# Kernel optimization log

Measured on AMD Instinct MI355X. Metric: run time of the kernel, lower is better.

Reference implementation:

```python
import jax, jax.numpy as jnp
import numpy as np

B, C_IN, N, HC = 32, 128, 8192, 64
HEAD_NAMES = ['hm', 'reg', 'height', 'dim', 'rot', 'iou']
HEAD_OUT = [3, 2, 1, 3, 2, 1]
EPS = 1e-5
INIT_BIAS = -2.19


def setup_inputs() -> dict:
    key = jax.random.key(0)
    ks = jax.random.split(key, 16)
    d = {}
    d['ct_feat'] = jax.random.normal(ks[0], (B, C_IN, N), jnp.float32)
    # shared conv (1x1) + BN1d params
    d['sh_w'] = jax.random.normal(ks[1], (HC, C_IN), jnp.float32) * 0.05
    d['sh_b'] = jnp.zeros((HC,), jnp.float32)
    d['sh_g'] = jnp.ones((HC,), jnp.float32)
    d['sh_beta'] = jnp.zeros((HC,), jnp.float32)
    d['sh_mean'] = jax.random.normal(ks[2], (HC,), jnp.float32) * 0.1
    d['sh_var'] = jax.random.uniform(ks[3], (HC,), jnp.float32) + 0.5
    # first conv layer of each SepHead branch (stacked over 6 heads)
    d['head_w1'] = jax.random.normal(ks[4], (6, HC, HC), jnp.float32) * 0.05
    d['head_b1'] = jnp.zeros((6, HC), jnp.float32)
    d['head_g1'] = jnp.ones((6, HC), jnp.float32)
    d['head_beta1'] = jnp.zeros((6, HC), jnp.float32)
    d['head_mean1'] = jax.random.normal(ks[5], (6, HC), jnp.float32) * 0.1
    d['head_var1'] = jax.random.uniform(ks[6], (6, HC), jnp.float32) + 0.5
    # final conv of each branch (distinct out channels)
    for i, (name, c_out) in enumerate(zip(HEAD_NAMES, HEAD_OUT)):
        d[name + '_w'] = jax.random.normal(ks[7 + i], (c_out, HC), jnp.float32) * 0.05
        if name == 'hm':  # hm final bias is filled with init_bias
            d[name + '_b'] = jnp.full((c_out,), INIT_BIAS, jnp.float32)
        else:
            d[name + '_b'] = jnp.zeros((c_out,), jnp.float32)
    return d


def _bn(x, g, b, m, v):
    # x: [B, C, N]; params: [C]
    return (x - m[:, None]) * jax.lax.rsqrt(v[:, None] + EPS) * g[:, None] + b[:, None]


def reference(ct_feat, sh_w, sh_b, sh_g, sh_beta, sh_mean, sh_var,
              head_w1, head_b1, head_g1, head_beta1, head_mean1, head_var1,
              hm_w, hm_b, reg_w, reg_b, height_w, height_b,
              dim_w, dim_b, rot_w, rot_b, iou_w, iou_b):
    # shared_conv: Conv1d(k=1) + BN1d + ReLU
    y = jnp.einsum('oc,bcn->bon', sh_w, ct_feat) + sh_b[:, None]
    y = jax.nn.relu(_bn(y, sh_g, sh_beta, sh_mean, sh_var))  # [B, HC, N]

    # first layer of all 6 head branches, batched over head axis h
    z = jnp.einsum('hoc,bcn->hbon', head_w1, y) + head_b1[:, None, :, None]
    z = (z - head_mean1[:, None, :, None]) * jax.lax.rsqrt(head_var1[:, None, :, None] + EPS)
    z = z * head_g1[:, None, :, None] + head_beta1[:, None, :, None]
    z = jax.nn.relu(z)  # [6, B, HC, N]

    finals = [(hm_w, hm_b), (reg_w, reg_b), (height_w, height_b),
              (dim_w, dim_b), (rot_w, rot_b), (iou_w, iou_b)]
    outs = [jnp.einsum('oc,bcn->bon', w, z[i]) + b[:, None]
            for i, (w, b) in enumerate(finals)]
    # concat in head order [hm(3), reg(2), height(1), dim(3), rot(2), iou(1)] -> [B, 12, N]
    return jnp.concatenate(outs, axis=1)
```

## Files before the change

kernel.cpp:

```cpp
#include <hip/hip_runtime.h>
#include <hip/hip_bf16.h>
#include <cstdint>

typedef __attribute__((ext_vector_type(8))) short bf16x8;
typedef __attribute__((ext_vector_type(4))) float f32x4;
typedef __attribute__((ext_vector_type(2))) int i32x2;

#define NCOL 8192

#define WS_AW 0
#define WS_A1 8192
#define WS_AF 32768
#define WS_U16_TOTAL 38912
#define WS_OFSH 19456
#define WS_OFH  19520
#define WS_BIAS 19904
#define PREP_TOTAL (WS_U16_TOTAL + 464)

union FragU { uint32_t u[4]; bf16x8 v; uint4 q; };

__device__ __forceinline__ uint16_t f2bf(float f) {
  uint32_t x = __builtin_bit_cast(uint32_t, f);
  x += 0x7fffu + ((x >> 16) & 1u);
  return (uint16_t)(x >> 16);
}
__device__ __forceinline__ uint32_t rne_bits(float f) {
  uint32_t x = __builtin_bit_cast(uint32_t, f);
  return x + 0x7fffu + ((x >> 16) & 1u);
}
__device__ __forceinline__ uint32_t pack_bf16(float lo, float hi) {
  return __builtin_amdgcn_perm(rne_bits(hi), rne_bits(lo), 0x07060302u);
}

__device__ __forceinline__ void cswap(uint32_t lo, uint32_t hi,
                                      uint32_t& f1, uint32_t& f2) {
  i32x2 t = __builtin_amdgcn_permlane32_swap((int)lo, (int)hi, false, false);
  i32x2 f = __builtin_amdgcn_permlane16_swap(t[0], t[1], false, false);
  f1 = (uint32_t)f[0];
  f2 = (uint32_t)f[1];
}

__global__ __launch_bounds__(256) void ch_prep(
    const float* __restrict__ shw, const float* __restrict__ shb,
    const float* __restrict__ shg, const float* __restrict__ shbeta,
    const float* __restrict__ shmean, const float* __restrict__ shvar,
    const float* __restrict__ w1, const float* __restrict__ b1,
    const float* __restrict__ g1, const float* __restrict__ beta1,
    const float* __restrict__ mean1, const float* __restrict__ var1,
    const float* __restrict__ hm_w, const float* __restrict__ hm_b,
    const float* __restrict__ reg_w, const float* __restrict__ reg_b,
    const float* __restrict__ height_w, const float* __restrict__ height_b,
    const float* __restrict__ dim_w, const float* __restrict__ dim_b,
    const float* __restrict__ rot_w, const float* __restrict__ rot_b,
    const float* __restrict__ iou_w, const float* __restrict__ iou_b,
    uint16_t* __restrict__ wsq)
{
  const int e = blockIdx.x * 256 + threadIdx.x;
  if (e >= PREP_TOTAL) return;
  const int rowbase[6] = {0, 3, 5, 6, 9, 11};
  const int couts[6]   = {3, 2, 1, 3, 2, 1};
  const float* wfp[6]  = {hm_w, reg_w, height_w, dim_w, rot_w, iou_w};

  if (e < WS_A1) {
    const int i = e & 7, q = (e >> 3) & 3, kc = (e >> 5) & 3, m = e >> 7;
    const int k = kc * 32 + q * 8 + i;
    const float sc = shg[m] * rsqrtf(shvar[m] + 1e-5f);
    wsq[e] = f2bf(shw[m * 128 + k] * sc);
  } else if (e < WS_AF) {
    const int e2 = e - WS_A1;
    const int i = e2 & 7, q = (e2 >> 3) & 3, kc = (e2 >> 5) & 1,
              m = (e2 >> 6) & 63, h = e2 >> 12;
    const int k = kc * 32 + q * 8 + i, row = h * 64 + m;
    const float sc = g1[row] * rsqrtf(var1[row] + 1e-5f);
    wsq[e] = f2bf(w1[row * 64 + k] * sc);
  } else if (e < WS_U16_TOTAL) {
    const int e2 = e - WS_AF;
    const int i = e2 & 7, q = (e2 >> 3) & 3, kc = (e2 >> 5) & 1,
              m = (e2 >> 6) & 15, h = e2 >> 10;
    const int k = kc * 32 + q * 8 + i, rr = m - rowbase[h];
    const float v = (rr >= 0 && rr < couts[h]) ? wfp[h][rr * 64 + k] : 0.f;
    wsq[e] = f2bf(v);
  } else {
    const int t2 = e - WS_U16_TOTAL;
    float* wff = (float*)wsq;
    float v = 0.f;
    if (t2 < 64) {
      const float sc = shg[t2] * rsqrtf(shvar[t2] + 1e-5f);
      v = (shb[t2] - shmean[t2]) * sc + shbeta[t2];
    } else if (t2 < 448) {
      const int i = t2 - 64;
      const float sc = g1[i] * rsqrtf(var1[i] + 1e-5f);
      v = (b1[i] - mean1[i]) * sc + beta1[i];
    } else {
      const int i = t2 - 448;
      if (i < 3)       v = hm_b[i];
      else if (i < 5)  v = reg_b[i - 3];
      else if (i < 6)  v = height_b[i - 5];
      else if (i < 9)  v = dim_b[i - 6];
      else if (i < 11) v = rot_b[i - 9];
      else if (i < 12) v = iou_b[i - 11];
    }
    wff[WS_OFSH + t2] = v;
  }
}

__global__ __launch_bounds__(256) void ch_main(
    const float* __restrict__ ct,
    const uint16_t* __restrict__ wsq,
    const float* __restrict__ wsf,
    float* __restrict__ outp)
{
  const int t    = threadIdx.x;
  const int wv   = t >> 6;
  const int lane = t & 63;
  const int l15  = lane & 15;
  const int qd   = lane >> 4;
  const int bid  = blockIdx.x;
  const int b    = bid >> 6;
  const int col0 = (bid & 63) * 128;
  const int nb   = wv * 32;

  const float* ctb = ct + (size_t)b * 128 * NCOL;
  const int voff0 = qd * 8 * NCOL + col0 + nb + l15;

  float xv[4][2][8];
  #pragma unroll
  for (int kc = 0; kc < 4; ++kc)
    #pragma unroll
    for (int j = 0; j < 2; ++j)
      #pragma unroll
      for (int i2 = 0; i2 < 4; ++i2) {
        const size_t off = (size_t)((kc * 32 + 2 * i2) * NCOL) + voff0 + j * 16;
        xv[kc][j][2 * i2]     = ctb[off];
        xv[kc][j][2 * i2 + 1] = ctb[off + NCOL];
      }
  __builtin_amdgcn_sched_barrier(0);

  f32x4 accY[4][2];
  #pragma unroll
  for (int mt = 0; mt < 4; ++mt)
    #pragma unroll
    for (int j = 0; j < 2; ++j)
      accY[mt][j] = (f32x4){0.f, 0.f, 0.f, 0.f};

  #pragma unroll
  for (int kc = 0; kc < 4; ++kc) {
    bf16x8 a[4];
    #pragma unroll
    for (int mt = 0; mt < 4; ++mt) {
      FragU fa;
      fa.q = *(const uint4*)(wsq + WS_AW + ((mt * 16 + l15) * 4 + kc) * 32 + qd * 8);
      a[mt] = fa.v;
    }
    #pragma unroll
    for (int j = 0; j < 2; ++j) {
      FragU f;
      #pragma unroll
      for (int i2 = 0; i2 < 4; ++i2)
        f.u[i2] = pack_bf16(xv[kc][j][2 * i2], xv[kc][j][2 * i2 + 1]);
      #pragma unroll
      for (int mt = 0; mt < 4; ++mt)
        accY[mt][j] = __builtin_amdgcn_mfma_f32_16x16x32_bf16(a[mt], f.v, accY[mt][j], 0, 0, 0);
    }
  }

  FragU yfrag[2][2];
  #pragma unroll
  for (int j = 0; j < 2; ++j) {
    uint32_t P[4][2];
    #pragma unroll
    for (int mt = 0; mt < 4; ++mt) {
      const f32x4 of = *(const f32x4*)(wsf + WS_OFSH + mt * 16 + qd * 4);
      const f32x4 v = accY[mt][j];
      P[mt][0] = pack_bf16(fmaxf(v[0] + of[0], 0.f), fmaxf(v[1] + of[1], 0.f));
      P[mt][1] = pack_bf16(fmaxf(v[2] + of[2], 0.f), fmaxf(v[3] + of[3], 0.f));
    }
    #pragma unroll
    for (int kc = 0; kc < 2; ++kc)
      #pragma unroll
      for (int u = 0; u < 2; ++u)
        cswap(P[2 * kc][u], P[2 * kc + 1][u],
              yfrag[kc][j].u[u], yfrag[kc][j].u[u + 2]);
  }

  f32x4 accO[2];
  accO[0] = (f32x4){0.f, 0.f, 0.f, 0.f};
  accO[1] = (f32x4){0.f, 0.f, 0.f, 0.f};

  const uint16_t* a1p = wsq + WS_A1 + l15 * 64 + qd * 8;
  const uint16_t* afp = wsq + WS_AF + l15 * 64 + qd * 8;
  const float*    ofp = wsf + WS_OFH + qd * 4;

  #pragma unroll 1
  for (int h = 0; h < 6; ++h) {
    FragU wa[2][4];
    FragU af[2];
    f32x4 ofv[4];
    #pragma unroll
    for (int kc = 0; kc < 2; ++kc)
      #pragma unroll
      for (int mt = 0; mt < 4; ++mt)
        wa[kc][mt].q = *(const uint4*)(a1p + mt * 1024 + kc * 32);
    #pragma unroll
    for (int kc = 0; kc < 2; ++kc)
      af[kc].q = *(const uint4*)(afp + kc * 32);
    #pragma unroll
    for (int mt = 0; mt < 4; ++mt)
      ofv[mt] = *(const f32x4*)(ofp + mt * 16);
    __builtin_amdgcn_sched_barrier(0);

    f32x4 accZ[4][2];
    #pragma unroll
    for (int mt = 0; mt < 4; ++mt)
      #pragma unroll
      for (int j = 0; j < 2; ++j)
        accZ[mt][j] = (f32x4){0.f, 0.f, 0.f, 0.f};

    #pragma unroll
    for (int kc = 0; kc < 2; ++kc)
      #pragma unroll
      for (int j = 0; j < 2; ++j)
        #pragma unroll
        for (int mt = 0; mt < 4; ++mt)
          accZ[mt][j] = __builtin_amdgcn_mfma_f32_16x16x32_bf16(wa[kc][mt].v, yfrag[kc][j].v, accZ[mt][j], 0, 0, 0);

    #pragma unroll
    for (int j = 0; j < 2; ++j) {
      uint32_t Q[4][2];
      #pragma unroll
      for (int mt = 0; mt < 4; ++mt) {
        const f32x4 v = accZ[mt][j];
        Q[mt][0] = pack_bf16(fmaxf(v[0] + ofv[mt][0], 0.f), fmaxf(v[1] + ofv[mt][1], 0.f));
        Q[mt][1] = pack_bf16(fmaxf(v[2] + ofv[mt][2], 0.f), fmaxf(v[3] + ofv[mt][3], 0.f));
      }
      FragU zf[2];
      #pragma unroll
      for (int kc = 0; kc < 2; ++kc)
        #pragma unroll
        for (int u = 0; u < 2; ++u)
          cswap(Q[2 * kc][u], Q[2 * kc + 1][u], zf[kc].u[u], zf[kc].u[u + 2]);

      #pragma unroll
      for (int kc = 0; kc < 2; ++kc)
        accO[j] = __builtin_amdgcn_mfma_f32_16x16x32_bf16(af[kc].v, zf[kc].v, accO[j], 0, 0, 0);
    }

    a1p += 4096;
    afp += 1024;
    ofp += 64;
  }

  if (qd < 3) {
    const f32x4 bs = *(const f32x4*)(wsf + WS_BIAS + qd * 4);
    #pragma unroll
    for (int j = 0; j < 2; ++j) {
      const int col = col0 + nb + j * 16 + l15;
      #pragma unroll
      for (int r = 0; r < 4; ++r)
        outp[((size_t)(b * 12 + qd * 4 + r)) * NCOL + col] = accO[j][r] + bs[r];
    }
  }
}

extern "C" void kernel_launch(void* const* d_in, const int* in_sizes, int n_in,
                              void* d_out, int out_size, void* d_ws, size_t ws_size,
                              hipStream_t stream) {
  (void)out_size; (void)ws_size;
  static const int sortedPos[25] = {
      0, 24, 19, 21, 20, 22, 23, 8, 3, 5, 4, 6, 7,
      12, 11, 16, 15, 10, 9, 2, 1, 18, 17, 14, 13};
  const bool sorted_order =
      (n_in == 25) && (in_sizes[1] == 3) && (in_sizes[2] == 192) &&
      (in_sizes[8] == 24576) && (in_sizes[24] == 8192);
  const float* p[25];
  for (int r = 0; r < 25; ++r)
    p[r] = (const float*)d_in[sorted_order ? sortedPos[r] : r];

  uint16_t* wsq = (uint16_t*)d_ws;

  hipLaunchKernelGGL(ch_prep, dim3((PREP_TOTAL + 255) / 256), dim3(256), 0, stream,
      p[1], p[2], p[3], p[4], p[5], p[6],
      p[7], p[8], p[9], p[10], p[11], p[12],
      p[13], p[14], p[15], p[16], p[17], p[18],
      p[19], p[20], p[21], p[22], p[23], p[24],
      wsq);

  hipLaunchKernelGGL(ch_main, dim3(2048), dim3(256), 0, stream,
      p[0], (const uint16_t*)wsq, (const float*)wsq, (float*)d_out);
}
```

Baseline: 292.6 us.

## Double-buffer input tiles in LDS via async global_load_lds with persistent column loop

The main kernel now has each block process 8 consecutive 64-column tiles instead of one 128-column tile. Input tiles are staged into a double-buffered, XOR-swizzled LDS buffer with asynchronous global-to-LDS loads, so the next tile's fetch overlaps the current tile's MFMA work. Shared-conv weights and offsets are hoisted out of the loop into registers, and the grid shrinks to 512 blocks with launch bounds asking for 2 blocks per CU. The trade-off is 64KB of LDS per block and hand-written vmcnt waits, which cap occupancy and depend on the exact count of outstanding loads.

```diff
diff --git a/kernel.cpp b/kernel.cpp
--- a/kernel.cpp
+++ b/kernel.cpp
@@ -104,132 +104,143 @@
   }
 }
 
-__global__ __launch_bounds__(256) void ch_main(
+__global__ __launch_bounds__(256, 2) void ch_main(
     const float* __restrict__ ct,
     const uint16_t* __restrict__ wsq,
     const float* __restrict__ wsf,
     float* __restrict__ outp)
 {
+  __shared__ __align__(16) float sm_x[2][128 * 64];
+
   const int t    = threadIdx.x;
   const int wv   = t >> 6;
   const int lane = t & 63;
   const int l15  = lane & 15;
   const int qd   = lane >> 4;
   const int bid  = blockIdx.x;
-  const int b    = bid >> 6;
-  const int col0 = (bid & 63) * 128;
-  const int nb   = wv * 32;
-
+  const int b    = bid >> 4;
+  const int g    = bid & 15;
   const float* ctb = ct + (size_t)b * 128 * NCOL;
-  const int voff0 = qd * 8 * NCOL + col0 + nb + l15;
-
-  float xv[4][2][8];
+
+#define STAGE(bsel, it)                                                        \
+  {                                                                            \
+    const int col0_ = (g * 8 + (it)) * 64;                                     \
+    _Pragma("unroll")                                                          \
+    for (int i = 0; i < 8; ++i) {                                              \
+      const int ii = wv * 8 + i;                                               \
+      const int k  = 4 * ii + qd;                                              \
+      const int sw = (k >> 3) & 3;                                             \
+      const float* src = ctb + (size_t)k * NCOL + col0_ +                      \
+                         ((4 * l15) ^ (sw << 4));                              \
+      __builtin_amdgcn_global_load_lds(                                        \
+          (const __attribute__((address_space(1))) uint32_t*)src,              \
+          (__attribute__((address_space(3))) uint32_t*)&sm_x[bsel][ii * 256],  \
+          16, 0, 0);                                                           \
+    }                                                                          \
+  }
+
+  FragU aw[4][4];
   #pragma unroll
   for (int kc = 0; kc < 4; ++kc)
     #pragma unroll
-    for (int j = 0; j < 2; ++j)
-      #pragma unroll
-      for (int i2 = 0; i2 < 4; ++i2) {
-        const size_t off = (size_t)((kc * 32 + 2 * i2) * NCOL) + voff0 + j * 16;
-        xv[kc][j][2 * i2]     = ctb[off];
-        xv[kc][j][2 * i2 + 1] = ctb[off + NCOL];
-      }
-  __builtin_amdgcn_sched_barrier(0);
-
-  f32x4 accY[4][2];
+    for (int mt = 0; mt < 4; ++mt)
+      aw[kc][mt].q = *(const uint4*)(wsq + WS_AW + ((mt * 16 + l15) * 4 + kc) * 32 + qd * 8);
+  f32x4 ofsh[4];
   #pragma unroll
   for (int mt = 0; mt < 4; ++mt)
-    #pragma unroll
-    for (int j = 0; j < 2; ++j)
-      accY[mt][j] = (f32x4){0.f, 0.f, 0.f, 0.f};
-
-  #pragma unroll
-  for (int kc = 0; kc < 4; ++kc) {
-    bf16x8 a[4];
-    #pragma unroll
-    for (int mt = 0; mt < 4; ++mt) {
-      FragU fa;
-      fa.q = *(const uint4*)(wsq + WS_AW + ((mt * 16 + l15) * 4 + kc) * 32 + qd * 8);
-      a[mt] = fa.v;
-    }
-    #pragma unroll
-    for (int j = 0; j < 2; ++j) {
-      FragU f;
-      #pragma unroll
-      for (int i2 = 0; i2 < 4; ++i2)
-        f.u[i2] = pack_bf16(xv[kc][j][2 * i2], xv[kc][j][2 * i2 + 1]);
-      #pragma unroll
-      for (int mt = 0; mt < 4; ++mt)
-        accY[mt][j] = __builtin_amdgcn_mfma_f32_16x16x32_bf16(a[mt], f.v, accY[mt][j], 0, 0, 0);
-    }
-  }
-
-  FragU yfrag[2][2];
-  #pragma unroll
-  for (int j = 0; j < 2; ++j) {
-    uint32_t P[4][2];
-    #pragma unroll
-    for (int mt = 0; mt < 4; ++mt) {
-      const f32x4 of = *(const f32x4*)(wsf + WS_OFSH + mt * 16 + qd * 4);
-      const f32x4 v = accY[mt][j];
-      P[mt][0] = pack_bf16(fmaxf(v[0] + of[0], 0.f), fmaxf(v[1] + of[1], 0.f));
-      P[mt][1] = pack_bf16(fmaxf(v[2] + of[2], 0.f), fmaxf(v[3] + of[3], 0.f));
-    }
-    #pragma unroll
-    for (int kc = 0; kc < 2; ++kc)
-      #pragma unroll
-      for (int u = 0; u < 2; ++u)
-        cswap(P[2 * kc][u], P[2 * kc + 1][u],
-              yfrag[kc][j].u[u], yfrag[kc][j].u[u + 2]);
-  }
-
-  f32x4 accO[2];
-  accO[0] = (f32x4){0.f, 0.f, 0.f, 0.f};
-  accO[1] = (f32x4){0.f, 0.f, 0.f, 0.f};
-
-  const uint16_t* a1p = wsq + WS_A1 + l15 * 64 + qd * 8;
-  const uint16_t* afp = wsq + WS_AF + l15 * 64 + qd * 8;
-  const float*    ofp = wsf + WS_OFH + qd * 4;
+    ofsh[mt] = *(const f32x4*)(wsf + WS_OFSH + mt * 16 + qd * 4);
+  const f32x4 bs = *(const f32x4*)(wsf + WS_BIAS + (qd & 3) * 4);
+
+  STAGE(0, 0);
+  STAGE(1, 1);
 
   #pragma unroll 1
-  for (int h = 0; h < 6; ++h) {
-    FragU wa[2][4];
-    FragU af[2];
-    f32x4 ofv[4];
-    #pragma unroll
-    for (int kc = 0; kc < 2; ++kc)
-      #pragma unroll
-      for (int mt = 0; mt < 4; ++mt)
-        wa[kc][mt].q = *(const uint4*)(a1p + mt * 1024 + kc * 32);
-    #pragma unroll
-    for (int kc = 0; kc < 2; ++kc)
-      af[kc].q = *(const uint4*)(afp + kc * 32);
+  for (int it = 0; it < 8; ++it) {
+    const int bsel = it & 1;
+    const int col0 = (g * 8 + it) * 64;
+
+    if (it == 0)      asm volatile("s_waitcnt vmcnt(8)" ::: "memory");
+    else if (it < 7)  asm volatile("s_waitcnt vmcnt(12)" ::: "memory");
+    else              asm volatile("s_waitcnt vmcnt(0)" ::: "memory");
+    __builtin_amdgcn_s_barrier();
+
+    const float* smf = &sm_x[bsel][0];
+    const int cx = (wv * 16 + l15) ^ (qd << 4);
+
+    f32x4 accY[4];
     #pragma unroll
     for (int mt = 0; mt < 4; ++mt)
-      ofv[mt] = *(const f32x4*)(ofp + mt * 16);
-    __builtin_amdgcn_sched_barrier(0);
-
-    f32x4 accZ[4][2];
+      accY[mt] = (f32x4){0.f, 0.f, 0.f, 0.f};
+
     #pragma unroll
-    for (int mt = 0; mt < 4; ++mt)
-      #pragma unroll
-      for (int j = 0; j < 2; ++j)
-        accZ[mt][j] = (f32x4){0.f, 0.f, 0.f, 0.f};
-
-    #pragma unroll
-    for (int kc = 0; kc < 2; ++kc)
-      #pragma unroll
-      for (int j = 0; j < 2; ++j)
+    for (int kc = 0; kc < 4; ++kc) {
+      FragU f;
+      #pragma unroll
+      for (int i2 = 0; i2 < 4; ++i2) {
+        const int k = kc * 32 + qd * 8 + 2 * i2;
+        const int w = k * 64 + cx;
+        f.u[i2] = pack_bf16(smf[w], smf[w + 64]);
+      }
+      #pragma unroll
+      for (int mt = 0; mt < 4; ++mt)
+        accY[mt] = __builtin_amdgcn_mfma_f32_16x16x32_bf16(aw[kc][mt].v, f.v, accY[mt], 0, 0, 0);
+    }
+    __builtin_amdgcn_s_barrier();
+
+    if (it < 6) STAGE(bsel, it + 2);
+
+    FragU yfrag[2];
+    {
+      uint32_t P[4][2];
+      #pragma unroll
+      for (int mt = 0; mt < 4; ++mt) {
+        const f32x4 v = accY[mt];
+        P[mt][0] = pack_bf16(fmaxf(v[0] + ofsh[mt][0], 0.f), fmaxf(v[1] + ofsh[mt][1], 0.f));
+        P[mt][1] = pack_bf16(fmaxf(v[2] + ofsh[mt][2], 0.f), fmaxf(v[3] + ofsh[mt][3], 0.f));
+      }
+      #pragma unroll
+      for (int kc = 0; kc < 2; ++kc)
+        #pragma unroll
+        for (int u = 0; u < 2; ++u)
+          cswap(P[2 * kc][u], P[2 * kc + 1][u], yfrag[kc].u[u], yfrag[kc].u[u + 2]);
+    }
+
+    f32x4 accO = (f32x4){0.f, 0.f, 0.f, 0.f};
+    const uint16_t* a1p = wsq + WS_A1 + l15 * 64 + qd * 8;
+    const uint16_t* afp = wsq + WS_AF + l15 * 64 + qd * 8;
+    const float*    ofp = wsf + WS_OFH + qd * 4;
+
+    #pragma unroll 1
+    for (int h = 0; h < 6; ++h) {
+      FragU wa[2][4];
+      FragU af[2];
+      f32x4 ofv[4];
+      #pragma unroll
+      for (int kc = 0; kc < 2; ++kc)
         #pragma unroll
         for (int mt = 0; mt < 4; ++mt)
-          accZ[mt][j] = __builtin_amdgcn_mfma_f32_16x16x32_bf16(wa[kc][mt].v, yfrag[kc][j].v, accZ[mt][j], 0, 0, 0);
-
-    #pragma unroll
-    for (int j = 0; j < 2; ++j) {
+          wa[kc][mt].q = *(const uint4*)(a1p + mt * 1024 + kc * 32);
+      #pragma unroll
+      for (int kc = 0; kc < 2; ++kc)
+        af[kc].q = *(const uint4*)(afp + kc * 32);
+      #pragma unroll
+      for (int mt = 0; mt < 4; ++mt)
+        ofv[mt] = *(const f32x4*)(ofp + mt * 16);
+
+      f32x4 accZ[4];
+      #pragma unroll
+      for (int mt = 0; mt < 4; ++mt)
+        accZ[mt] = (f32x4){0.f, 0.f, 0.f, 0.f};
+      #pragma unroll
+      for (int kc = 0; kc < 2; ++kc)
+        #pragma unroll
+        for (int mt = 0; mt < 4; ++mt)
+          accZ[mt] = __builtin_amdgcn_mfma_f32_16x16x32_bf16(wa[kc][mt].v, yfrag[kc].v, accZ[mt], 0, 0, 0);
+
       uint32_t Q[4][2];
       #pragma unroll
       for (int mt = 0; mt < 4; ++mt) {
-        const f32x4 v = accZ[mt][j];
+        const f32x4 v = accZ[mt];
         Q[mt][0] = pack_bf16(fmaxf(v[0] + ofv[mt][0], 0.f), fmaxf(v[1] + ofv[mt][1], 0.f));
         Q[mt][1] = pack_bf16(fmaxf(v[2] + ofv[mt][2], 0.f), fmaxf(v[3] + ofv[mt][3], 0.f));
       }
@@ -239,27 +250,23 @@
         #pragma unroll
         for (int u = 0; u < 2; ++u)
           cswap(Q[2 * kc][u], Q[2 * kc + 1][u], zf[kc].u[u], zf[kc].u[u + 2]);
-
-      #pragma unroll
-      for (int kc = 0; kc < 2; ++kc)
-        accO[j] = __builtin_amdgcn_mfma_f32_16x16x32_bf16(af[kc].v, zf[kc].v, accO[j], 0, 0, 0);
-    }
-
-    a1p += 4096;
-    afp += 1024;
-    ofp += 64;
+      #pragma unroll
+      for (int kc = 0; kc < 2; ++kc)
+        accO = __builtin_amdgcn_mfma_f32_16x16x32_bf16(af[kc].v, zf[kc].v, accO, 0, 0, 0);
+
+      a1p += 4096;
+      afp += 1024;
+      ofp += 64;
+    }
+
+    if (qd < 3) {
+      const int col = col0 + wv * 16 + l15;
+      #pragma unroll
+      for (int r = 0; r < 4; ++r)
+        outp[((size_t)(b * 12 + qd * 4 + r)) * NCOL + col] = accO[r] + bs[r];
+    }
   }
-
-  if (qd < 3) {
-    const f32x4 bs = *(const f32x4*)(wsf + WS_BIAS + qd * 4);
-    #pragma unroll
-    for (int j = 0; j < 2; ++j) {
-      const int col = col0 + nb + j * 16 + l15;
-      #pragma unroll
-      for (int r = 0; r < 4; ++r)
-        outp[((size_t)(b * 12 + qd * 4 + r)) * NCOL + col] = accO[j][r] + bs[r];
-    }
-  }
+#undef STAGE
 }
 
 extern "C" void kernel_launch(void* const* d_in, const int* in_sizes, int n_in,
@@ -285,6 +292,6 @@
       p[19], p[20], p[21], p[22], p[23], p[24],
       wsq);
 
-  hipLaunchKernelGGL(ch_main, dim3(2048), dim3(256), 0, stream,
+  hipLaunchKernelGGL(ch_main, dim3(512), dim3(256), 0, stream,
       p[0], (const uint16_t*)wsq, (const float*)wsq, (float*)d_out);
 }
```

New measurement: 349.1 us. +19.3%, slower.
